# Kernel tuning notes

Measured on AMD Instinct MI355X. Metric: run time of the kernel, lower is better.

The kernel has to match this reference:

```python
import jax, jax.numpy as jnp
import numpy as np

ROTARY_DIM = 32
THETA = 10000.0

def _rotate_half(t):
    # interleaved pairs: (..., d) -> rotate each (x1, x2) pair to (-x2, x1)
    x = t.reshape(t.shape[:-1] + (-1, 2))
    x1, x2 = x[..., 0], x[..., 1]
    return jnp.stack([-x2, x1], axis=-1).reshape(t.shape)

def _apply_rope(t, offset=0):
    # t: (B, h, T, dh); rotate only the first ROTARY_DIM dims
    T = t.shape[-2]
    inv_freq = 1.0 / (THETA ** (jnp.arange(0, ROTARY_DIM, 2, dtype=jnp.float32) / ROTARY_DIM))
    pos = jnp.arange(T, dtype=jnp.float32) + offset
    freqs = pos[:, None] * inv_freq[None, :]                 # (T, ROTARY_DIM/2)
    freqs = jnp.repeat(freqs, 2, axis=-1)                    # (T, ROTARY_DIM) interleaved
    cos, sin = jnp.cos(freqs), jnp.sin(freqs)
    t_rot, t_pass = t[..., :ROTARY_DIM], t[..., ROTARY_DIM:]
    t_rot = t_rot * cos + _rotate_half(t_rot) * sin
    return jnp.concatenate([t_rot, t_pass], axis=-1)

def setup_inputs() -> dict:
    key = jax.random.key(0)
    k1, k2, k3 = jax.random.split(key, 3)
    B, T, dim = 4, 1024, 1024
    x = jax.random.normal(k1, (B, T, dim), dtype=jnp.float32)
    Wqkv = jax.random.normal(k2, (dim, 3 * dim), dtype=jnp.float32) * (dim ** -0.5)
    Wout = jax.random.normal(k3, (dim, dim), dtype=jnp.float32) * (dim ** -0.5)
    return {"x": x, "Wqkv": Wqkv, "Wout": Wout}

def reference(x, Wqkv, Wout):
    B, T, dim = x.shape
    n_heads = 16
    dh = dim // n_heads
    qkv = x @ Wqkv                                            # (B, T, 3*dim)
    qkv = qkv.reshape(B, T, 3, n_heads, dh)
    qkv = jnp.transpose(qkv, (2, 0, 3, 1, 4))                 # (3, B, h, T, dh)
    q, k, v = qkv[0], qkv[1], qkv[2]
    q = _apply_rope(q, offset=0)
    k = _apply_rope(k, offset=0)
    scale = 1.0 / jnp.sqrt(jnp.asarray(dh, dtype=x.dtype))
    scores = jnp.einsum('bhqd,bhkd->bhqk', q, k) * scale      # (B, h, T, T)
    causal = jnp.tril(jnp.ones((T, T), dtype=bool))
    scores = jnp.where(causal, scores, jnp.asarray(-jnp.inf, dtype=scores.dtype))
    attn = jax.nn.softmax(scores, axis=-1)
    out = jnp.einsum('bhqk,bhkd->bhqd', attn, v)              # (B, h, T, dh)
    out = jnp.transpose(out, (0, 2, 1, 3)).reshape(B, T, dim)
    return out @ Wout
```

## Files before the change

kernel.cpp:

```cpp
#include <hip/hip_runtime.h>
#include <cstdint>
#include <cstddef>

typedef __bf16 bf16;
typedef __bf16 bf16x4 __attribute__((ext_vector_type(4)));
typedef __bf16 bf16x8 __attribute__((ext_vector_type(8)));
typedef float f32x4 __attribute__((ext_vector_type(4)));

#define DEVINL __device__ __forceinline__

static constexpr int Tn   = 1024;
static constexpr int DIM  = 1024;
static constexpr int NH   = 16;
static constexpr int DH   = 64;
static constexpr int QKVN = 3072;

DEVINL void g2l16(const void* g, void* l) {
  __builtin_amdgcn_global_load_lds(
      (const __attribute__((address_space(1))) void*)g,
      (__attribute__((address_space(3))) void*)l, 16, 0, 0);
}


__global__ void k_convert_and_tab(const float* __restrict__ in, bf16* __restrict__ out,
                                  float2* __restrict__ tab) {
  if (blockIdx.x >= 4096) {
    int e = (blockIdx.x - 4096) * 256 + threadIdx.x;
    int t = e >> 4, fi = e & 15;
    float inv = exp2f(-(float)fi * 0.830482023721841f);
    float sn, cs;
    sincosf((float)t * inv, &sn, &cs);
    tab[e] = make_float2(cs, sn);
    return;
  }
  int i = blockIdx.x * blockDim.x + threadIdx.x;
  float4 v = reinterpret_cast<const float4*>(in)[i];
  bf16 o[4] = {(bf16)v.x, (bf16)v.y, (bf16)v.z, (bf16)v.w};
  reinterpret_cast<uint2*>(out)[i] = *reinterpret_cast<uint2*>(o);
}

__global__ void k_transpose_w2(const float* __restrict__ w1, bf16* __restrict__ o1,
                               const float* __restrict__ w2, bf16* __restrict__ o2) {
  __shared__ float tile[32][33];
  const bool second = blockIdx.x >= 96;
  const float* in = second ? w2 : w1;
  bf16* out = second ? o2 : o1;
  const int N = second ? 1024 : 3072;
  int n0 = (second ? (blockIdx.x - 96) : blockIdx.x) * 32, k0 = blockIdx.y * 32;
  int tx = threadIdx.x, ty = threadIdx.y;
#pragma unroll
  for (int j = 0; j < 32; j += 8)
    tile[ty + j][tx] = in[(size_t)(k0 + ty + j) * N + n0 + tx];
  __syncthreads();
#pragma unroll
  for (int j = 0; j < 32; j += 8)
    out[(size_t)(n0 + ty + j) * 1024 + k0 + tx] = (bf16)tile[tx][ty + j];
}

template <bool F32OUT, int BN, bool ROPE>
__global__ __launch_bounds__(256) void k_gemm_bt(
    const bf16* __restrict__ A, const bf16* __restrict__ Bt,
    void* __restrict__ Cp, bf16* __restrict__ vt, const float2* __restrict__ tab,
    int M, int N, int K) {
  constexpr int NI = BN / 32;
  __shared__ bf16 As[128 * 64];
  __shared__ bf16 Bs[BN * 64];
  const int tid  = threadIdx.x;
  const int wave = tid >> 6, lane = tid & 63;
  const int lrow = lane & 15, quad = lane >> 4;
  const int m0 = blockIdx.y * 128, n0 = blockIdx.x * BN;
  const int wm = (wave >> 1) * 64, wn = (wave & 1) * (BN / 2);

  f32x4 acc[4][NI];
#pragma unroll
  for (int mi = 0; mi < 4; mi++)
#pragma unroll
    for (int ni = 0; ni < NI; ni++) acc[mi][ni] = 0.f;

  for (int k0 = 0; k0 < K; k0 += 64) {
    __syncthreads();
#pragma unroll
    for (int i = 0; i < 4; i++) {
      int li = i * 256 + tid;
      int row = li >> 3, c = li & 7;
      int gc = c ^ (row & 7);
      g2l16(A + (size_t)(m0 + row) * K + k0 + gc * 8, As + li * 8);
    }
#pragma unroll
    for (int i = 0; i < BN / 32; i++) {
      int li = i * 256 + tid;
      int row = li >> 3, c = li & 7;
      int gc = c ^ (row & 7);
      g2l16(Bt + (size_t)(n0 + row) * K + k0 + gc * 8, Bs + li * 8);
    }
    __syncthreads();
#pragma unroll
    for (int ki = 0; ki < 2; ki++) {
      bf16x8 af[4], bfr[NI];
#pragma unroll
      for (int mi = 0; mi < 4; mi++) {
        int r = wm + mi * 16 + lrow;
        int pc = (ki * 4 + quad) ^ (r & 7);
        af[mi] = *reinterpret_cast<const bf16x8*>(As + r * 64 + pc * 8);
      }
#pragma unroll
      for (int ni = 0; ni < NI; ni++) {
        int r = wn + ni * 16 + lrow;
        int pc = (ki * 4 + quad) ^ (r & 7);
        bfr[ni] = *reinterpret_cast<const bf16x8*>(Bs + r * 64 + pc * 8);
      }
#pragma unroll
      for (int mi = 0; mi < 4; mi++)
#pragma unroll
        for (int ni = 0; ni < NI; ni++)
          acc[mi][ni] = __builtin_amdgcn_mfma_f32_16x16x32_bf16(af[mi], bfr[ni], acc[mi][ni], 0, 0, 0);
    }
  }

#pragma unroll
  for (int mi = 0; mi < 4; mi++)
#pragma unroll
    for (int ni = 0; ni < NI; ni++) {
      int col = n0 + wn + ni * 16 + lrow;
      if (ROPE && col >= 2 * DIM) {
        int hd = col - 2 * DIM;
        int row0 = m0 + wm + mi * 16 + quad * 4;
        bf16x4 pk;
#pragma unroll
        for (int r = 0; r < 4; r++) pk[r] = (bf16)acc[mi][ni][r];
        *reinterpret_cast<bf16x4*>(
            vt + ((size_t)(((row0 >> 10) << 10) + hd) << 10) + (row0 & (Tn - 1))) = pk;
        continue;
      }
      bool rot = false;
      int fi = 0;
      if (ROPE) {
        rot = (col & 63) < 32;
        fi = (col >> 1) & 15;
      }
#pragma unroll
      for (int r = 0; r < 4; r++) {
        int row = m0 + wm + mi * 16 + quad * 4 + r;
        float v = acc[mi][ni][r];
        if (ROPE && rot) {
          float pv = __shfl_xor(v, 1, 64);
          float2 cs = tab[((row & (Tn - 1)) << 4) + fi];
          v = (col & 1) ? (v * cs.x + pv * cs.y) : (v * cs.x - pv * cs.y);
        }
        if (F32OUT)
          reinterpret_cast<float*>(Cp)[(size_t)row * N + col] = v;
        else
          reinterpret_cast<bf16*>(Cp)[(size_t)row * N + col] = (bf16)v;
      }
    }
}

__global__ __launch_bounds__(256) void k_attn(
    const bf16* __restrict__ qkv, const bf16* __restrict__ vt,
    bf16* __restrict__ ao) {
  __shared__ bf16 Ks[2][64 * 64];
  __shared__ bf16 Vs[2][64 * 64];
  __shared__ bf16 Ps[4][16 * 64];

  const int tid  = threadIdx.x;
  const int wave = tid >> 6, lane = tid & 63;
  const int lrow = lane & 15, quad = lane >> 4;
  const int bh = blockIdx.y, b = bh >> 4, h = bh & 15;
  const int jn = blockIdx.x;
  const int jf = 15 - jn;
  const int qwf = jf * 64 + wave * 16;
  const int qwn = jn * 64 + wave * 16;
  const size_t qbase = (size_t)b * Tn * QKVN;

  bf16x8 qff[2], qfn[2];
  {
    const float SC = 0.125f * 1.44269504088896f;
    const bf16* qpf = qkv + qbase + (size_t)(qwf + lrow) * QKVN + h * DH;
    const bf16* qpn = qkv + qbase + (size_t)(qwn + lrow) * QKVN + h * DH;
    qff[0] = *reinterpret_cast<const bf16x8*>(qpf + quad * 8);
    qff[1] = *reinterpret_cast<const bf16x8*>(qpf + 32 + quad * 8);
    qfn[0] = *reinterpret_cast<const bf16x8*>(qpn + quad * 8);
    qfn[1] = *reinterpret_cast<const bf16x8*>(qpn + 32 + quad * 8);
#pragma unroll
    for (int j = 0; j < 8; j++) {
      qff[0][j] = (bf16)((float)qff[0][j] * SC);
      qff[1][j] = (bf16)((float)qff[1][j] * SC);
      qfn[0][j] = (bf16)((float)qfn[0][j] * SC);
      qfn[1][j] = (bf16)((float)qfn[1][j] * SC);
    }
  }

  f32x4 oaf[4], oan[4];
#pragma unroll
  for (int g = 0; g < 4; g++) { oaf[g] = 0.f; oan[g] = 0.f; }
  float lif = 0.f, lin = 0.f;

  const int ntiles = jf + 1;

  auto stage = [&](int k0, int bufi) {
#pragma unroll
    for (int i = 0; i < 2; i++) {
      int li2 = i * 256 + tid;
      int row = li2 >> 3, c = li2 & 7;
      int gc = c ^ (row & 7);
      g2l16(qkv + qbase + (size_t)(k0 + row) * QKVN + DIM + h * DH + gc * 8,
            &Ks[bufi][li2 * 8]);
      g2l16(vt + ((size_t)bh * DH + row) * Tn + k0 + gc * 8,
            &Vs[bufi][li2 * 8]);
    }
  };

  auto unit = [&](const bf16* ks, const bf16* vs, bf16x8 (&qf)[2], f32x4 (&oa)[4],
                  float& li, bool diag) {
    f32x4 s[4];
#pragma unroll
    for (int g = 0; g < 4; g++) s[g] = 0.f;
#pragma unroll
    for (int kh = 0; kh < 2; kh++) {
      const int cX = ((kh * 4 + quad) ^ (lrow & 7)) << 3;
#pragma unroll
      for (int g = 0; g < 4; g++) {
        bf16x8 kf = *reinterpret_cast<const bf16x8*>(ks + (g * 16 + lrow) * 64 + cX);
        s[g] = __builtin_amdgcn_mfma_f32_16x16x32_bf16(kf, qf[kh], s[g], 0, 0, 0);
      }
    }
    float psum = 0.f;
    const int qrel = wave * 16 + lrow;
#pragma unroll
    for (int g = 0; g < 4; g++) {
      bf16x4 pk;
#pragma unroll
      for (int r = 0; r < 4; r++) {
        float p = exp2f(s[g][r]);
        if (diag) {
          int kl = g * 16 + quad * 4 + r;
          p = (kl <= qrel) ? p : 0.f;
        }
        psum += p;
        pk[r] = (bf16)p;
      }
      int chunk = 2 * g + (quad >> 1);
      *reinterpret_cast<bf16x4*>(
          Ps[wave] + lrow * 64 + ((chunk ^ (lrow & 7)) << 3) + 4 * (quad & 1)) = pk;
    }
    li += psum;
#pragma unroll
    for (int kh = 0; kh < 2; kh++) {
      const int cX = ((kh * 4 + quad) ^ (lrow & 7)) << 3;
      bf16x8 pf = *reinterpret_cast<const bf16x8*>(Ps[wave] + lrow * 64 + cX);
#pragma unroll
      for (int g = 0; g < 4; g++) {
        bf16x8 vf = *reinterpret_cast<const bf16x8*>(vs + (g * 16 + lrow) * 64 + cX);
        oa[g] = __builtin_amdgcn_mfma_f32_16x16x32_bf16(pf, vf, oa[g], 0, 0, 0);
      }
    }
  };

  stage(0, 0);

  for (int kt = 0; kt < ntiles; kt++) {
    const int buf = kt & 1;
    __syncthreads();
    if (kt + 1 < ntiles) stage((kt + 1) << 6, buf ^ 1);

    const bf16* ks = Ks[buf];
    const bf16* vs = Vs[buf];

    unit(ks, vs, qff, oaf, lif, kt == jf);
    if (kt <= jn)
      unit(ks, vs, qfn, oan, lin, kt == jn);
  }

  lif += __shfl_xor(lif, 16, 64); lif += __shfl_xor(lif, 32, 64);
  lin += __shfl_xor(lin, 16, 64); lin += __shfl_xor(lin, 32, 64);

#pragma unroll
  for (int r = 0; r < 4; r++) {
    int m = quad * 4 + r;
    float invf = 1.0f / __shfl(lif, m, 64);
    float invn = 1.0f / __shfl(lin, m, 64);
    bf16* dstf = ao + ((size_t)b * Tn + qwf + m) * DIM + h * DH;
    bf16* dstn = ao + ((size_t)b * Tn + qwn + m) * DIM + h * DH;
    dstf[ 0 + lrow] = (bf16)(oaf[0][r] * invf);
    dstf[16 + lrow] = (bf16)(oaf[1][r] * invf);
    dstf[32 + lrow] = (bf16)(oaf[2][r] * invf);
    dstf[48 + lrow] = (bf16)(oaf[3][r] * invf);
    dstn[ 0 + lrow] = (bf16)(oan[0][r] * invn);
    dstn[16 + lrow] = (bf16)(oan[1][r] * invn);
    dstn[32 + lrow] = (bf16)(oan[2][r] * invn);
    dstn[48 + lrow] = (bf16)(oan[3][r] * invn);
  }
}

extern "C" void kernel_launch(void* const* d_in, const int* in_sizes, int n_in,
                              void* d_out, int out_size, void* d_ws, size_t ws_size,
                              hipStream_t stream) {
  const float* x    = (const float*)d_in[0];
  const float* Wqkv = (const float*)d_in[1];
  const float* Wout = (const float*)d_in[2];
  char* ws = (char*)d_ws;

  bf16*   xb    = (bf16*)(ws + 0);
  bf16*   wqkvT = (bf16*)(ws + 8388608);
  bf16*   woutT = (bf16*)(ws + 14680064);
  bf16*   qkv   = (bf16*)(ws + 16777216);
  bf16*   vt    = (bf16*)(ws + 41943040);
  bf16*   ao    = (bf16*)(ws + 50331648);
  float2* tab   = (float2*)(ws + 58720256);

  k_convert_and_tab<<<4160, 256, 0, stream>>>(x, xb, tab);
  k_transpose_w2<<<dim3(128, 32), dim3(32, 8), 0, stream>>>(Wqkv, wqkvT, Wout, woutT);
  k_gemm_bt<false, 128, true><<<dim3(24, 32), 256, 0, stream>>>(
      xb, wqkvT, (void*)qkv, vt, tab, 4096, 3072, 1024);
  k_attn<<<dim3(8, 64), 256, 0, stream>>>(qkv, vt, ao);
  k_gemm_bt<true, 64, false><<<dim3(16, 32), 256, 0, stream>>>(
      ao, woutT, d_out, nullptr, nullptr, 4096, 1024, 1024);
  (void)in_sizes; (void)n_in; (void)out_size; (void)ws_size;
}
```

Baseline: 173.7 us.

## Merge prep kernels, hoist GEMM load pointers, swap MFMA operands for row-vector epilogue

Combines the activation conversion, RoPE table and weight transposes into one launch, which removes a kernel boundary. The GEMM precomputes its global load pointers once and advances them each k-step, dropping per-iteration address arithmetic. Swapping the MFMA operands transposes the accumulator layout, so each lane holds four consecutive columns. That lets the epilogue apply RoPE pairwise inside a lane without shuffles and emit vectorized row stores for q/k and the output. The cost is that the V-transpose path now writes scalar, strided bf16 values instead of a packed 4-wide store.

```diff
diff --git a/kernel.cpp b/kernel.cpp
--- a/kernel.cpp
+++ b/kernel.cpp
@@ -21,11 +21,21 @@
       (__attribute__((address_space(3))) void*)l, 16, 0, 0);
 }
 
-
-__global__ void k_convert_and_tab(const float* __restrict__ in, bf16* __restrict__ out,
-                                  float2* __restrict__ tab) {
-  if (blockIdx.x >= 4096) {
-    int e = (blockIdx.x - 4096) * 256 + threadIdx.x;
+__global__ void k_prep(const float* __restrict__ x, bf16* __restrict__ xb,
+                       float2* __restrict__ tab,
+                       const float* __restrict__ w1, bf16* __restrict__ o1,
+                       const float* __restrict__ w2, bf16* __restrict__ o2) {
+  __shared__ float tile[32][33];
+  int bx = blockIdx.x;
+  if (bx < 4096) {
+    int i = bx * 256 + threadIdx.x;
+    float4 v = reinterpret_cast<const float4*>(x)[i];
+    bf16 o[4] = {(bf16)v.x, (bf16)v.y, (bf16)v.z, (bf16)v.w};
+    reinterpret_cast<uint2*>(xb)[i] = *reinterpret_cast<uint2*>(o);
+    return;
+  }
+  if (bx < 4160) {
+    int e = (bx - 4096) * 256 + threadIdx.x;
     int t = e >> 4, fi = e & 15;
     float inv = exp2f(-(float)fi * 0.830482023721841f);
     float sn, cs;
@@ -33,21 +43,11 @@
     tab[e] = make_float2(cs, sn);
     return;
   }
-  int i = blockIdx.x * blockDim.x + threadIdx.x;
-  float4 v = reinterpret_cast<const float4*>(in)[i];
-  bf16 o[4] = {(bf16)v.x, (bf16)v.y, (bf16)v.z, (bf16)v.w};
-  reinterpret_cast<uint2*>(out)[i] = *reinterpret_cast<uint2*>(o);
-}
-
-__global__ void k_transpose_w2(const float* __restrict__ w1, bf16* __restrict__ o1,
-                               const float* __restrict__ w2, bf16* __restrict__ o2) {
-  __shared__ float tile[32][33];
-  const bool second = blockIdx.x >= 96;
-  const float* in = second ? w2 : w1;
-  bf16* out = second ? o2 : o1;
-  const int N = second ? 1024 : 3072;
-  int n0 = (second ? (blockIdx.x - 96) : blockIdx.x) * 32, k0 = blockIdx.y * 32;
-  int tx = threadIdx.x, ty = threadIdx.y;
+  int sub = bx - 4160;
+  const float* in; bf16* out; int N, n0, k0;
+  if (sub < 3072) { in = w1; out = o1; N = 3072; n0 = (sub % 96) * 32; k0 = (sub / 96) * 32; }
+  else { sub -= 3072; in = w2; out = o2; N = 1024; n0 = (sub & 31) * 32; k0 = (sub >> 5) * 32; }
+  int tx = threadIdx.x & 31, ty = threadIdx.x >> 5;
 #pragma unroll
   for (int j = 0; j < 32; j += 8)
     tile[ty + j][tx] = in[(size_t)(k0 + ty + j) * N + n0 + tx];
@@ -63,6 +63,7 @@
     void* __restrict__ Cp, bf16* __restrict__ vt, const float2* __restrict__ tab,
     int M, int N, int K) {
   constexpr int NI = BN / 32;
+  constexpr int NB = BN / 32;
   __shared__ bf16 As[128 * 64];
   __shared__ bf16 Bs[BN * 64];
   const int tid  = threadIdx.x;
@@ -71,6 +72,21 @@
   const int m0 = blockIdx.y * 128, n0 = blockIdx.x * BN;
   const int wm = (wave >> 1) * 64, wn = (wave & 1) * (BN / 2);
 
+  const bf16* aP[4];
+  const bf16* bP[NB];
+#pragma unroll
+  for (int i = 0; i < 4; i++) {
+    int li = i * 256 + tid;
+    int row = li >> 3, c = li & 7, gc = c ^ (row & 7);
+    aP[i] = A + (size_t)(m0 + row) * K + gc * 8;
+  }
+#pragma unroll
+  for (int i = 0; i < NB; i++) {
+    int li = i * 256 + tid;
+    int row = li >> 3, c = li & 7, gc = c ^ (row & 7);
+    bP[i] = Bt + (size_t)(n0 + row) * K + gc * 8;
+  }
+
   f32x4 acc[4][NI];
 #pragma unroll
   for (int mi = 0; mi < 4; mi++)
@@ -81,17 +97,13 @@
     __syncthreads();
 #pragma unroll
     for (int i = 0; i < 4; i++) {
-      int li = i * 256 + tid;
-      int row = li >> 3, c = li & 7;
-      int gc = c ^ (row & 7);
-      g2l16(A + (size_t)(m0 + row) * K + k0 + gc * 8, As + li * 8);
-    }
-#pragma unroll
-    for (int i = 0; i < BN / 32; i++) {
-      int li = i * 256 + tid;
-      int row = li >> 3, c = li & 7;
-      int gc = c ^ (row & 7);
-      g2l16(Bt + (size_t)(n0 + row) * K + k0 + gc * 8, Bs + li * 8);
+      g2l16(aP[i], As + (i * 256 + tid) * 8);
+      aP[i] += 64;
+    }
+#pragma unroll
+    for (int i = 0; i < NB; i++) {
+      g2l16(bP[i], Bs + (i * 256 + tid) * 8);
+      bP[i] += 64;
     }
     __syncthreads();
 #pragma unroll
@@ -113,46 +125,47 @@
       for (int mi = 0; mi < 4; mi++)
 #pragma unroll
         for (int ni = 0; ni < NI; ni++)
-          acc[mi][ni] = __builtin_amdgcn_mfma_f32_16x16x32_bf16(af[mi], bfr[ni], acc[mi][ni], 0, 0, 0);
-    }
-  }
-
-#pragma unroll
-  for (int mi = 0; mi < 4; mi++)
+          acc[mi][ni] = __builtin_amdgcn_mfma_f32_16x16x32_bf16(bfr[ni], af[mi], acc[mi][ni], 0, 0, 0);
+    }
+  }
+
+#pragma unroll
+  for (int mi = 0; mi < 4; mi++) {
+    const int row = m0 + wm + mi * 16 + lrow;
 #pragma unroll
     for (int ni = 0; ni < NI; ni++) {
-      int col = n0 + wn + ni * 16 + lrow;
-      if (ROPE && col >= 2 * DIM) {
-        int hd = col - 2 * DIM;
-        int row0 = m0 + wm + mi * 16 + quad * 4;
+      const int colb = n0 + wn + ni * 16 + quad * 4;
+      f32x4 v = acc[mi][ni];
+      if (ROPE && n0 >= 2 * DIM) {
+        int t = row & (Tn - 1), bb = row >> 10;
+        int hdb = colb - 2 * DIM;
+#pragma unroll
+        for (int r = 0; r < 4; r++)
+          vt[((size_t)((bb << 10) + hdb + r) << 10) + t] = (bf16)v[r];
+        continue;
+      }
+      if (ROPE && ((colb & 63) < 32)) {
+        int t = row & (Tn - 1);
+        int fi0 = (colb >> 1) & 15;
+        float2 c0 = tab[(t << 4) + fi0];
+        float2 c1 = tab[(t << 4) + fi0 + 1];
+        float a0 = v[0], a1 = v[1], a2 = v[2], a3 = v[3];
+        v[0] = a0 * c0.x - a1 * c0.y;
+        v[1] = a1 * c0.x + a0 * c0.y;
+        v[2] = a2 * c1.x - a3 * c1.y;
+        v[3] = a3 * c1.x + a2 * c1.y;
+      }
+      if (F32OUT) {
+        float4 st = {v[0], v[1], v[2], v[3]};
+        *reinterpret_cast<float4*>(reinterpret_cast<float*>(Cp) + (size_t)row * N + colb) = st;
+      } else {
         bf16x4 pk;
 #pragma unroll
-        for (int r = 0; r < 4; r++) pk[r] = (bf16)acc[mi][ni][r];
-        *reinterpret_cast<bf16x4*>(
-            vt + ((size_t)(((row0 >> 10) << 10) + hd) << 10) + (row0 & (Tn - 1))) = pk;
-        continue;
-      }
-      bool rot = false;
-      int fi = 0;
-      if (ROPE) {
-        rot = (col & 63) < 32;
-        fi = (col >> 1) & 15;
-      }
-#pragma unroll
-      for (int r = 0; r < 4; r++) {
-        int row = m0 + wm + mi * 16 + quad * 4 + r;
-        float v = acc[mi][ni][r];
-        if (ROPE && rot) {
-          float pv = __shfl_xor(v, 1, 64);
-          float2 cs = tab[((row & (Tn - 1)) << 4) + fi];
-          v = (col & 1) ? (v * cs.x + pv * cs.y) : (v * cs.x - pv * cs.y);
-        }
-        if (F32OUT)
-          reinterpret_cast<float*>(Cp)[(size_t)row * N + col] = v;
-        else
-          reinterpret_cast<bf16*>(Cp)[(size_t)row * N + col] = (bf16)v;
-      }
-    }
+        for (int r = 0; r < 4; r++) pk[r] = (bf16)v[r];
+        *reinterpret_cast<bf16x4*>(reinterpret_cast<bf16*>(Cp) + (size_t)row * N + colb) = pk;
+      }
+    }
+  }
 }
 
 __global__ __launch_bounds__(256) void k_attn(
@@ -308,8 +321,7 @@
   bf16*   ao    = (bf16*)(ws + 50331648);
   float2* tab   = (float2*)(ws + 58720256);
 
-  k_convert_and_tab<<<4160, 256, 0, stream>>>(x, xb, tab);
-  k_transpose_w2<<<dim3(128, 32), dim3(32, 8), 0, stream>>>(Wqkv, wqkvT, Wout, woutT);
+  k_prep<<<8256, 256, 0, stream>>>(x, xb, tab, Wqkv, wqkvT, Wout, woutT);
   k_gemm_bt<false, 128, true><<<dim3(24, 32), 256, 0, stream>>>(
       xb, wqkvT, (void*)qkv, vt, tab, 4096, 3072, 1024);
   k_attn<<<dim3(8, 64), 256, 0, stream>>>(qkv, vt, ao);
```

New measurement: 160.7 us. -7.5%, faster.
